# Kernel optimization log

Measured on AMD Instinct MI355X. Metric: run time of the kernel, lower is better.

Reference implementation:

```python
import jax, jax.numpy as jnp
import numpy as np

LN_EPS = 1e-5

def _ln(x, w, b):
    mu = jnp.mean(x, axis=-1, keepdims=True)
    var = jnp.var(x, axis=-1, keepdims=True)
    return (x - mu) * jax.lax.rsqrt(var + LN_EPS) * w + b

def setup_inputs() -> dict:
    key = jax.random.key(0)
    ks = jax.random.split(key, 16)
    B, T, N = 32, 1024, 77
    D, TD, TE = 512, 256, 2048
    s = lambda fan: 1.0 / np.sqrt(fan)
    return {
        "x": jax.random.normal(ks[0], (B, T, D), jnp.float32),
        "xf": jax.random.normal(ks[1], (B, N, TD), jnp.float32),
        "emb": jax.random.normal(ks[2], (B, TE), jnp.float32),
        "src_mask": jnp.ones((B, T), jnp.float32),
        "cond_type": jax.random.randint(ks[3], (B,), 0, 100, jnp.int64),
        "norm_w": jnp.ones((D,), jnp.float32),
        "norm_b": jnp.zeros((D,), jnp.float32),
        "tnorm_w": jnp.ones((TD,), jnp.float32),
        "tnorm_b": jnp.zeros((TD,), jnp.float32),
        "Wq": jax.random.normal(ks[4], (D, D), jnp.float32) * s(D),
        "bq": jnp.zeros((D,), jnp.float32),
        "Wk": jax.random.normal(ks[5], (D, TD), jnp.float32) * s(TD),
        "bk": jnp.zeros((D,), jnp.float32),
        "Wv": jax.random.normal(ks[6], (D, TD), jnp.float32) * s(TD),
        "bv": jnp.zeros((D,), jnp.float32),
        "emb_w": jax.random.normal(ks[7], (2 * D, TE), jnp.float32) * s(TE),
        "emb_b": jnp.zeros((2 * D,), jnp.float32),
        "snorm_w": jnp.ones((D,), jnp.float32),
        "snorm_b": jnp.zeros((D,), jnp.float32),
        "Wout": jax.random.normal(ks[8], (D, D), jnp.float32) * s(D),
        "bout": jnp.zeros((D,), jnp.float32),
    }

def reference(x, xf, emb, src_mask, cond_type,
              norm_w, norm_b, tnorm_w, tnorm_b,
              Wq, bq, Wk, bk, Wv, bv,
              emb_w, emb_b, snorm_w, snorm_b, Wout, bout):
    B, T, D = x.shape
    N = xf.shape[1]
    H = 8
    dh = D // H
    # projections (no 1/sqrt(dh) scaling, per original)
    q = (_ln(x, norm_w, norm_b) @ Wq.T + bq).reshape(B, T, H, dh)
    xf_n = _ln(xf, tnorm_w, tnorm_b)
    k = (xf_n @ Wk.T + bk).reshape(B, N, H, dh)
    # cond_type gating: text_cond_type = (cond_type % 10 > 0)
    tc = (cond_type % 10 > 0).astype(x.dtype)  # [B]
    bias = (1.0 - tc)[:, None, None, None] * -1000000.0  # [B,1,1,1]
    attn = jnp.einsum('bthd,bnhd->btnh', q, k) + bias
    attn = jax.nn.softmax(attn, axis=2)  # over keys N
    v = (xf_n @ Wv.T + bv) * tc[:, None, None]
    v = v.reshape(B, N, H, dh)
    y = jnp.einsum('btnh,bnhd->bthd', attn, v).reshape(B, T, D)
    # StylizationBlock: silu->linear on emb -> scale/shift, ln, silu->linear, residual
    e = jax.nn.silu(emb) @ emb_w.T + emb_b  # [B, 2D]
    scale, shift = jnp.split(e[:, None, :], 2, axis=2)  # [B,1,D] each
    h = _ln(y, snorm_w, snorm_b) * (1.0 + scale) + shift
    h = jax.nn.silu(h) @ Wout.T + bout
    return x + h
```

## Files before the change

kernel.cpp:

```cpp
#include <hip/hip_runtime.h>
#include <math.h>

#define B_   32
#define T_   1024
#define N_   77
#define D_   512
#define TD_  256
#define TE_  2048
#define H_   8
#define DH_  64

typedef short bf16x8 __attribute__((ext_vector_type(8)));
typedef float f32x4  __attribute__((ext_vector_type(4)));

__device__ __forceinline__ float sigmoidf_fast(float x) {
    return 1.0f / (1.0f + __expf(-x));
}

__device__ __forceinline__ unsigned short f2b(float f) {
    unsigned int u = __float_as_uint(f);
    unsigned int r = u + 0x7FFFu + ((u >> 16) & 1u);
    return (unsigned short)(r >> 16);
}

#define GL16(g, l) __builtin_amdgcn_global_load_lds(                         \
    (const __attribute__((address_space(1))) unsigned int*)(g),              \
    (__attribute__((address_space(3))) unsigned int*)(l), 16, 0, 0)

__global__ __launch_bounds__(256) void ln_rows_kernel(
    const float* __restrict__ x, const float* __restrict__ w, const float* __restrict__ b,
    float* __restrict__ out, int rows, int cols)
{
    int wave = blockIdx.x * 4 + (threadIdx.x >> 6);
    int lane = threadIdx.x & 63;
    if (wave >= rows) return;
    const float* row = x + (size_t)wave * cols;
    float s = 0.f, ss = 0.f;
    for (int c = lane; c < cols; c += 64) {
        float v = row[c];
        s += v; ss += v * v;
    }
    #pragma unroll
    for (int off = 32; off; off >>= 1) {
        s  += __shfl_xor(s, off);
        ss += __shfl_xor(ss, off);
    }
    float m = s / cols;
    float var = ss / cols - m * m;
    float r = rsqrtf(var + 1e-5f);
    float* orow = out + (size_t)wave * cols;
    for (int c = lane; c < cols; c += 64) {
        orow[c] = (row[c] - m) * r * w[c] + b[c];
    }
}

template <int MODE>
__global__ __launch_bounds__(256) void gemm_kernel(
    const float* __restrict__ A, const float* __restrict__ W,
    const float* __restrict__ bias,
    const int*   __restrict__ cond,
    float* __restrict__ C,
    int M, int NN, int K)
{
    const int tx = threadIdx.x & 15;
    const int ty = threadIdx.x >> 4;
    const int m0 = blockIdx.y * 64;
    const int n0 = blockIdx.x * 64;

    __shared__ float As[16][68];
    __shared__ float Ws[16][68];

    float acc[4][4] = {};

    for (int k0 = 0; k0 < K; k0 += 16) {
        int kk = k0 + tx;
        #pragma unroll
        for (int p = 0; p < 4; p++) {
            int row = ty + p * 16;
            int m = m0 + row;
            int mc = m < M ? m : (M - 1);
            As[tx][row] = A[(size_t)mc * K + kk];
        }
        #pragma unroll
        for (int p = 0; p < 4; p++) {
            int nn = ty + p * 16;
            Ws[tx][nn] = W[(size_t)(n0 + nn) * K + kk];
        }
        __syncthreads();
        #pragma unroll
        for (int cc = 0; cc < 16; cc++) {
            float4 av = *(const float4*)&As[cc][ty * 4];
            float4 wv = *(const float4*)&Ws[cc][tx * 4];
            float a4[4] = {av.x, av.y, av.z, av.w};
            float w4[4] = {wv.x, wv.y, wv.z, wv.w};
            #pragma unroll
            for (int i = 0; i < 4; i++)
                #pragma unroll
                for (int j = 0; j < 4; j++)
                    acc[i][j] = fmaf(a4[i], w4[j], acc[i][j]);
        }
        __syncthreads();
    }

    #pragma unroll
    for (int i = 0; i < 4; i++) {
        int m = m0 + ty * 4 + i;
        if (m >= M) continue;
        float rowscale = 1.f;
        if (MODE == 3) {
            int b3 = m / N_;
            rowscale = ((cond[b3] % 10) > 0) ? 1.f : 0.f;
        }
        #pragma unroll
        for (int j = 0; j < 4; j++) {
            int n = n0 + tx * 4 + j;
            float o = acc[i][j] + bias[n];
            if (MODE == 3) o *= rowscale;
            C[(size_t)m * NN + n] = o;
        }
    }
}

__global__ __launch_bounds__(256) void f32_to_bf16_kernel(
    const float* __restrict__ src, unsigned short* __restrict__ dst)
{
    int idx = (blockIdx.x * 256 + threadIdx.x) * 8;
    float4 v0 = *(const float4*)(src + idx);
    float4 v1 = *(const float4*)(src + idx + 4);
    ushort4 o0 = {f2b(v0.x), f2b(v0.y), f2b(v0.z), f2b(v0.w)};
    ushort4 o1 = {f2b(v1.x), f2b(v1.y), f2b(v1.z), f2b(v1.w)};
    *(ushort4*)(dst + idx)     = o0;
    *(ushort4*)(dst + idx + 4) = o1;
}

__global__ __launch_bounds__(256) void silu_kernel(
    const float* __restrict__ src, float* __restrict__ dst)
{
    int idx = (blockIdx.x * 256 + threadIdx.x) * 4;
    float4 v = *(const float4*)(src + idx);
    v.x = v.x * sigmoidf_fast(v.x);
    v.y = v.y * sigmoidf_fast(v.y);
    v.z = v.z * sigmoidf_fast(v.z);
    v.w = v.w * sigmoidf_fast(v.w);
    *(float4*)(dst + idx) = v;
}

__global__ __launch_bounds__(256) void emb_gemm_kernel(
    const float* __restrict__ se, const float* __restrict__ W,
    float* __restrict__ e)
{
    int wid = blockIdx.x * 4 + (threadIdx.x >> 6);
    int lane = threadIdx.x & 63;
    int ngrp = wid >> 3;
    int bgrp = wid & 7;

    float acc[4][4] = {};
    #pragma unroll 2
    for (int it = 0; it < 8; it++) {
        int k = (it * 64 + lane) * 4;
        float4 sv[4], wv[4];
        #pragma unroll
        for (int bi = 0; bi < 4; bi++)
            sv[bi] = *(const float4*)&se[(size_t)(bgrp * 4 + bi) * TE_ + k];
        #pragma unroll
        for (int ni = 0; ni < 4; ni++)
            wv[ni] = *(const float4*)&W[(size_t)(ngrp * 4 + ni) * TE_ + k];
        #pragma unroll
        for (int bi = 0; bi < 4; bi++)
            #pragma unroll
            for (int ni = 0; ni < 4; ni++) {
                acc[bi][ni] = fmaf(sv[bi].x, wv[ni].x, acc[bi][ni]);
                acc[bi][ni] = fmaf(sv[bi].y, wv[ni].y, acc[bi][ni]);
                acc[bi][ni] = fmaf(sv[bi].z, wv[ni].z, acc[bi][ni]);
                acc[bi][ni] = fmaf(sv[bi].w, wv[ni].w, acc[bi][ni]);
            }
    }
    #pragma unroll
    for (int bi = 0; bi < 4; bi++)
        #pragma unroll
        for (int ni = 0; ni < 4; ni++) {
            float a = acc[bi][ni];
            #pragma unroll
            for (int off = 32; off; off >>= 1) a += __shfl_xor(a, off);
            if (lane == 0)
                e[(size_t)(bgrp * 4 + bi) * 1024 + ngrp * 4 + ni] = a;
        }
}

__global__ __launch_bounds__(256) void prep_q_kernel(
    const float* __restrict__ x, const float* __restrict__ w, const float* __restrict__ b,
    unsigned short* __restrict__ outb)
{
    int row = blockIdx.x * 4 + (threadIdx.x >> 6);
    int lane = threadIdx.x & 63;
    const float* rp = x + (size_t)row * D_ + lane * 8;
    float4 v0 = *(const float4*)rp;
    float4 v1 = *(const float4*)(rp + 4);
    float s  = v0.x + v0.y + v0.z + v0.w + v1.x + v1.y + v1.z + v1.w;
    float ss = v0.x*v0.x + v0.y*v0.y + v0.z*v0.z + v0.w*v0.w
             + v1.x*v1.x + v1.y*v1.y + v1.z*v1.z + v1.w*v1.w;
    #pragma unroll
    for (int off = 32; off; off >>= 1) {
        s  += __shfl_xor(s, off);
        ss += __shfl_xor(ss, off);
    }
    float m = s * (1.f / D_);
    float r = rsqrtf(ss * (1.f / D_) - m * m + 1e-5f);
    float4 w0 = *(const float4*)(w + lane * 8);
    float4 w1 = *(const float4*)(w + lane * 8 + 4);
    float4 b0 = *(const float4*)(b + lane * 8);
    float4 b1 = *(const float4*)(b + lane * 8 + 4);
    ushort4 o0, o1;
    o0.x = f2b((v0.x - m) * r * w0.x + b0.x);
    o0.y = f2b((v0.y - m) * r * w0.y + b0.y);
    o0.z = f2b((v0.z - m) * r * w0.z + b0.z);
    o0.w = f2b((v0.w - m) * r * w0.w + b0.w);
    o1.x = f2b((v1.x - m) * r * w1.x + b1.x);
    o1.y = f2b((v1.y - m) * r * w1.y + b1.y);
    o1.z = f2b((v1.z - m) * r * w1.z + b1.z);
    o1.w = f2b((v1.w - m) * r * w1.w + b1.w);
    unsigned short* op = outb + (size_t)row * D_ + lane * 8;
    *(ushort4*)op       = o0;
    *(ushort4*)(op + 4) = o1;
}

__global__ __launch_bounds__(256) void prep_h_kernel(
    const float* __restrict__ y, const float* __restrict__ w, const float* __restrict__ b,
    const float* __restrict__ e, const float* __restrict__ emb_b,
    unsigned short* __restrict__ outb)
{
    int row = blockIdx.x * 4 + (threadIdx.x >> 6);
    int lane = threadIdx.x & 63;
    int bb = row >> 10;
    const float* rp = y + (size_t)row * D_ + lane * 8;
    float4 v0 = *(const float4*)rp;
    float4 v1 = *(const float4*)(rp + 4);
    float s  = v0.x + v0.y + v0.z + v0.w + v1.x + v1.y + v1.z + v1.w;
    float ss = v0.x*v0.x + v0.y*v0.y + v0.z*v0.z + v0.w*v0.w
             + v1.x*v1.x + v1.y*v1.y + v1.z*v1.z + v1.w*v1.w;
    #pragma unroll
    for (int off = 32; off; off >>= 1) {
        s  += __shfl_xor(s, off);
        ss += __shfl_xor(ss, off);
    }
    float m = s * (1.f / D_);
    float r = rsqrtf(ss * (1.f / D_) - m * m + 1e-5f);
    float4 w0 = *(const float4*)(w + lane * 8);
    float4 w1 = *(const float4*)(w + lane * 8 + 4);
    float4 b0 = *(const float4*)(b + lane * 8);
    float4 b1 = *(const float4*)(b + lane * 8 + 4);
    const float* ep = e + (size_t)bb * 1024 + lane * 8;
    float4 sc0 = *(const float4*)ep;
    float4 sc1 = *(const float4*)(ep + 4);
    float4 sh0 = *(const float4*)(ep + 512);
    float4 sh1 = *(const float4*)(ep + 512 + 4);
    float4 eb0 = *(const float4*)(emb_b + lane * 8);
    float4 eb1 = *(const float4*)(emb_b + lane * 8 + 4);
    float4 fb0 = *(const float4*)(emb_b + 512 + lane * 8);
    float4 fb1 = *(const float4*)(emb_b + 512 + lane * 8 + 4);
    sc0.x += eb0.x; sc0.y += eb0.y; sc0.z += eb0.z; sc0.w += eb0.w;
    sc1.x += eb1.x; sc1.y += eb1.y; sc1.z += eb1.z; sc1.w += eb1.w;
    sh0.x += fb0.x; sh0.y += fb0.y; sh0.z += fb0.z; sh0.w += fb0.w;
    sh1.x += fb1.x; sh1.y += fb1.y; sh1.z += fb1.z; sh1.w += fb1.w;
    float hv[8];
    hv[0] = ((v0.x - m) * r * w0.x + b0.x) * (1.f + sc0.x) + sh0.x;
    hv[1] = ((v0.y - m) * r * w0.y + b0.y) * (1.f + sc0.y) + sh0.y;
    hv[2] = ((v0.z - m) * r * w0.z + b0.z) * (1.f + sc0.z) + sh0.z;
    hv[3] = ((v0.w - m) * r * w0.w + b0.w) * (1.f + sc0.w) + sh0.w;
    hv[4] = ((v1.x - m) * r * w1.x + b1.x) * (1.f + sc1.x) + sh1.x;
    hv[5] = ((v1.y - m) * r * w1.y + b1.y) * (1.f + sc1.y) + sh1.y;
    hv[6] = ((v1.z - m) * r * w1.z + b1.z) * (1.f + sc1.z) + sh1.z;
    hv[7] = ((v1.w - m) * r * w1.w + b1.w) * (1.f + sc1.w) + sh1.w;
    ushort4 o0, o1;
    o0.x = f2b(hv[0] * sigmoidf_fast(hv[0]));
    o0.y = f2b(hv[1] * sigmoidf_fast(hv[1]));
    o0.z = f2b(hv[2] * sigmoidf_fast(hv[2]));
    o0.w = f2b(hv[3] * sigmoidf_fast(hv[3]));
    o1.x = f2b(hv[4] * sigmoidf_fast(hv[4]));
    o1.y = f2b(hv[5] * sigmoidf_fast(hv[5]));
    o1.z = f2b(hv[6] * sigmoidf_fast(hv[6]));
    o1.w = f2b(hv[7] * sigmoidf_fast(hv[7]));
    unsigned short* op = outb + (size_t)row * D_ + lane * 8;
    *(ushort4*)op       = o0;
    *(ushort4*)(op + 4) = o1;
}

template <int RESID, int OUTBF>
__global__ __launch_bounds__(256) void gemm_bf16_kernel(
    const unsigned short* __restrict__ Ab,
    const unsigned short* __restrict__ Wb,
    const float* __restrict__ bias,
    const float* __restrict__ resid,
    void* __restrict__ Cv)
{
    constexpr int K = 512;
    __shared__ __align__(16) unsigned short As[128 * 32];
    __shared__ __align__(16) unsigned short Bs[128 * 32];

    const int tid  = threadIdx.x;
    const int m0   = blockIdx.y * 128;
    const int n0   = blockIdx.x * 128;
    const int lane = tid & 63;
    const int w    = tid >> 6;
    const int l15  = lane & 15;
    const int quad = lane >> 4;
    const int wm   = (w >> 1) * 64;
    const int wn   = (w & 1) * 64;

    const int row_a = tid >> 2;
    const int col16 = tid & 3;

    f32x4 acc[4][4];
    #pragma unroll
    for (int i = 0; i < 4; i++)
        #pragma unroll
        for (int j = 0; j < 4; j++)
            acc[i][j] = (f32x4){0.f, 0.f, 0.f, 0.f};

    const char* gAbase = (const char*)Ab + ((size_t)(m0 + row_a) * K) * 2 + col16 * 16;
    const char* gBbase = (const char*)Wb + ((size_t)(n0 + row_a) * K) * 2 + col16 * 16;
    char* lA = (char*)As + tid * 16;
    char* lB = (char*)Bs + tid * 16;

    for (int k0 = 0; k0 < K; k0 += 32) {
        const char* gA = gAbase + k0 * 2;
        const char* gB = gBbase + k0 * 2;
        GL16(gA, lA);
        GL16(gA + (size_t)64 * K * 2, lA + 4096);
        GL16(gB, lB);
        GL16(gB + (size_t)64 * K * 2, lB + 4096);
        __syncthreads();

        bf16x8 af[4], bfr[4];
        #pragma unroll
        for (int i = 0; i < 4; i++)
            af[i] = *(const bf16x8*)&As[(wm + i * 16 + l15) * 32 + quad * 8];
        #pragma unroll
        for (int j = 0; j < 4; j++)
            bfr[j] = *(const bf16x8*)&Bs[(wn + j * 16 + l15) * 32 + quad * 8];
        #pragma unroll
        for (int i = 0; i < 4; i++)
            #pragma unroll
            for (int j = 0; j < 4; j++)
                acc[i][j] = __builtin_amdgcn_mfma_f32_16x16x32_bf16(af[i], bfr[j], acc[i][j], 0, 0, 0);
        __syncthreads();
    }

    float* C = (float*)Cv;
    unsigned short* Cb = (unsigned short*)Cv;
    #pragma unroll
    for (int i = 0; i < 4; i++) {
        int mbase = m0 + wm + i * 16 + quad * 4;
        #pragma unroll
        for (int j = 0; j < 4; j++) {
            int n = n0 + wn + j * 16 + l15;
            float bn = bias[n];
            #pragma unroll
            for (int r = 0; r < 4; r++) {
                size_t off = (size_t)(mbase + r) * 512 + n;
                float v = acc[i][j][r] + bn;
                if (RESID) v += resid[off];
                if (OUTBF) Cb[off] = f2b(v);
                else       C[off]  = v;
            }
        }
    }
}

#define QS_OFF 0
#define KS_OFF 4608
#define VT_OFF 10368
#define PS_OFF 17024
#define SMEM_SH 23680

__global__ __launch_bounds__(256) void attn_mfma_kernel(
    const unsigned short* __restrict__ qb,
    const float* __restrict__ kbuf, const float* __restrict__ vbuf,
    float* __restrict__ yout)
{
    __shared__ __align__(16) unsigned short smem[SMEM_SH];

    const int tid = threadIdx.x;
    const int t0 = blockIdx.x * 64;
    const int h  = blockIdx.y;
    const int b  = blockIdx.z;

    const unsigned short* qbase = qb + ((size_t)(b * T_ + t0)) * D_ + h * 64;
    #pragma unroll
    for (int i = 0; i < 2; i++) {
        int idx = tid + i * 256;
        int row = idx >> 3, c8 = idx & 7;
        bf16x8 v = *(const bf16x8*)(qbase + (size_t)row * D_ + c8 * 8);
        *(bf16x8*)&smem[QS_OFF + row * 72 + c8 * 8] = v;
    }
    const float* kbase = kbuf + (size_t)(b * N_) * D_ + h * 64;
    #pragma unroll
    for (int i = 0; i < 5; i++) {
        int idx = tid + i * 256;
        if (idx < N_ * 16) {
            int row = idx >> 4, c4 = idx & 15;
            float4 v = *(const float4*)(kbase + (size_t)row * D_ + c4 * 4);
            ushort4 o;
            o.x = f2b(v.x); o.y = f2b(v.y); o.z = f2b(v.z); o.w = f2b(v.w);
            *(ushort4*)&smem[KS_OFF + row * 72 + c4 * 4] = o;
        }
    }
    if (tid < 48) {
        int row = N_ + tid / 16, c4 = tid & 15;
        ushort4 z = {0, 0, 0, 0};
        *(ushort4*)&smem[KS_OFF + row * 72 + c4 * 4] = z;
    }
    const float* vbase = vbuf + (size_t)(b * N_) * D_ + h * 64;
    #pragma unroll
    for (int i = 0; i < 5; i++) {
        int idx = tid + i * 256;
        if (idx < N_ * 16) {
            int n = idx >> 4, c4 = idx & 15;
            float4 v = *(const float4*)(vbase + (size_t)n * D_ + c4 * 4);
            smem[VT_OFF + (c4 * 4 + 0) * 104 + n] = f2b(v.x);
            smem[VT_OFF + (c4 * 4 + 1) * 104 + n] = f2b(v.y);
            smem[VT_OFF + (c4 * 4 + 2) * 104 + n] = f2b(v.z);
            smem[VT_OFF + (c4 * 4 + 3) * 104 + n] = f2b(v.w);
        }
    }
    #pragma unroll
    for (int i = 0; i < 5; i++) {
        int idx = tid + i * 256;
        if (idx < 64 * 19) {
            int d = idx / 19, n = N_ + idx % 19;
            smem[VT_OFF + d * 104 + n] = 0;
        }
    }
    #pragma unroll
    for (int i = 0; i < 4; i++) {
        int idx = tid + i * 256;
        int row = idx >> 4, col = 80 + (idx & 15);
        smem[PS_OFF + row * 104 + col] = 0;
    }
    __syncthreads();

    const int lane = tid & 63;
    const int w    = tid >> 6;
    const int l15  = lane & 15;
    const int quad = lane >> 4;
    const int koff = quad * 8;
    const int mrow = w * 16 + l15;

    bf16x8 aq0 = *(const bf16x8*)&smem[QS_OFF + mrow * 72 + koff];
    bf16x8 aq1 = *(const bf16x8*)&smem[QS_OFF + mrow * 72 + 32 + koff];

    float s[5][4];
    #pragma unroll
    for (int nt = 0; nt < 5; nt++) {
        bf16x8 bk0 = *(const bf16x8*)&smem[KS_OFF + (nt * 16 + l15) * 72 + koff];
        bf16x8 bk1 = *(const bf16x8*)&smem[KS_OFF + (nt * 16 + l15) * 72 + 32 + koff];
        f32x4 c = {0.f, 0.f, 0.f, 0.f};
        c = __builtin_amdgcn_mfma_f32_16x16x32_bf16(aq0, bk0, c, 0, 0, 0);
        c = __builtin_amdgcn_mfma_f32_16x16x32_bf16(aq1, bk1, c, 0, 0, 0);
        #pragma unroll
        for (int r = 0; r < 4; r++) s[nt][r] = c[r];
    }
    if (l15 >= N_ - 64) {
        #pragma unroll
        for (int r = 0; r < 4; r++) s[4][r] = -1e30f;
    }
    float li[4];
    #pragma unroll
    for (int r = 0; r < 4; r++) {
        float m = s[0][r];
        #pragma unroll
        for (int nt = 1; nt < 5; nt++) m = fmaxf(m, s[nt][r]);
        m = fmaxf(m, __shfl_xor(m, 1));
        m = fmaxf(m, __shfl_xor(m, 2));
        m = fmaxf(m, __shfl_xor(m, 4));
        m = fmaxf(m, __shfl_xor(m, 8));
        float l = 0.f;
        #pragma unroll
        for (int nt = 0; nt < 5; nt++) {
            float ev = __expf(s[nt][r] - m);
            s[nt][r] = ev;
            l += ev;
        }
        l += __shfl_xor(l, 1);
        l += __shfl_xor(l, 2);
        l += __shfl_xor(l, 4);
        l += __shfl_xor(l, 8);
        li[r] = 1.f / l;
    }
    #pragma unroll
    for (int r = 0; r < 4; r++) {
        int prow = w * 16 + quad * 4 + r;
        #pragma unroll
        for (int nt = 0; nt < 5; nt++) {
            smem[PS_OFF + prow * 104 + nt * 16 + l15] = f2b(s[nt][r] * li[r]);
        }
    }

    bf16x8 pa0 = *(const bf16x8*)&smem[PS_OFF + mrow * 104 + 0  + koff];
    bf16x8 pa1 = *(const bf16x8*)&smem[PS_OFF + mrow * 104 + 32 + koff];
    bf16x8 pa2 = *(const bf16x8*)&smem[PS_OFF + mrow * 104 + 64 + koff];

    float* obase = yout + ((size_t)(b * T_ + t0 + w * 16)) * D_ + h * 64;
    #pragma unroll
    for (int dt = 0; dt < 4; dt++) {
        bf16x8 bv0 = *(const bf16x8*)&smem[VT_OFF + (dt * 16 + l15) * 104 + 0  + koff];
        bf16x8 bv1 = *(const bf16x8*)&smem[VT_OFF + (dt * 16 + l15) * 104 + 32 + koff];
        bf16x8 bv2 = *(const bf16x8*)&smem[VT_OFF + (dt * 16 + l15) * 104 + 64 + koff];
        f32x4 c = {0.f, 0.f, 0.f, 0.f};
        c = __builtin_amdgcn_mfma_f32_16x16x32_bf16(pa0, bv0, c, 0, 0, 0);
        c = __builtin_amdgcn_mfma_f32_16x16x32_bf16(pa1, bv1, c, 0, 0, 0);
        c = __builtin_amdgcn_mfma_f32_16x16x32_bf16(pa2, bv2, c, 0, 0, 0);
        #pragma unroll
        for (int r = 0; r < 4; r++) {
            obase[(size_t)(quad * 4 + r) * D_ + dt * 16 + l15] = c[r];
        }
    }
}

extern "C" void kernel_launch(void* const* d_in, const int* in_sizes, int n_in,
                              void* d_out, int out_size, void* d_ws, size_t ws_size,
                              hipStream_t stream)
{
    const float* x       = (const float*)d_in[0];
    const float* xf      = (const float*)d_in[1];
    const float* emb     = (const float*)d_in[2];
    const int*   cond    = (const int*)d_in[4];
    const float* norm_w  = (const float*)d_in[5];
    const float* norm_b  = (const float*)d_in[6];
    const float* tnorm_w = (const float*)d_in[7];
    const float* tnorm_b = (const float*)d_in[8];
    const float* Wq      = (const float*)d_in[9];
    const float* bq      = (const float*)d_in[10];
    const float* Wk      = (const float*)d_in[11];
    const float* bk      = (const float*)d_in[12];
    const float* Wv      = (const float*)d_in[13];
    const float* bv      = (const float*)d_in[14];
    const float* emb_w   = (const float*)d_in[15];
    const float* emb_b   = (const float*)d_in[16];
    const float* snorm_w = (const float*)d_in[17];
    const float* snorm_b = (const float*)d_in[18];
    const float* Wout    = (const float*)d_in[19];
    const float* bout    = (const float*)d_in[20];
    float* out = (float*)d_out;

    float* ws = (float*)d_ws;
    float* qy   = ws;
    float* xfn  = qy   + (size_t)B_ * T_ * D_;
    float* kbuf = xfn  + (size_t)B_ * N_ * TD_;
    float* vbuf = kbuf + (size_t)B_ * N_ * D_;
    float* ebuf = vbuf + (size_t)B_ * N_ * D_;
    float* sebuf= ebuf + (size_t)B_ * 2 * D_;
    unsigned short* abh = (unsigned short*)(sebuf + (size_t)B_ * TE_);
    unsigned short* wqb = abh + (size_t)B_ * T_ * D_;
    unsigned short* wob = wqb + (size_t)D_ * D_;
    unsigned short* qb  = (unsigned short*)d_out;

    const int BT = B_ * T_;
    const int BN = B_ * N_;

    ln_rows_kernel<<<(BN + 3) / 4, 256, 0, stream>>>(xf, tnorm_w, tnorm_b, xfn, BN, TD_);
    {
        dim3 grid(D_ / 64, (BN + 63) / 64);
        gemm_kernel<2><<<grid, 256, 0, stream>>>(xfn, Wk, bk, nullptr, kbuf, BN, D_, TD_);
    }
    {
        dim3 grid(D_ / 64, (BN + 63) / 64);
        gemm_kernel<3><<<grid, 256, 0, stream>>>(xfn, Wv, bv, cond, vbuf, BN, D_, TD_);
    }
    f32_to_bf16_kernel<<<128, 256, 0, stream>>>(Wq, wqb);
    f32_to_bf16_kernel<<<128, 256, 0, stream>>>(Wout, wob);
    prep_q_kernel<<<BT / 4, 256, 0, stream>>>(x, norm_w, norm_b, abh);
    {
        dim3 grid(D_ / 128, BT / 128);
        gemm_bf16_kernel<0, 1><<<grid, 256, 0, stream>>>(abh, wqb, bq, nullptr, qb);
    }
    silu_kernel<<<(B_ * TE_) / 1024, 256, 0, stream>>>(emb, sebuf);
    emb_gemm_kernel<<<512, 256, 0, stream>>>(sebuf, emb_w, ebuf);
    {
        dim3 grid(T_ / 64, H_, B_);
        attn_mfma_kernel<<<grid, 256, 0, stream>>>(qb, kbuf, vbuf, qy);
    }
    prep_h_kernel<<<BT / 4, 256, 0, stream>>>(qy, snorm_w, snorm_b, ebuf, emb_b, abh);
    {
        dim3 grid(D_ / 128, BT / 128);
        gemm_bf16_kernel<1, 0><<<grid, 256, 0, stream>>>(abh, wob, bout, x, out);
    }
}
```

Before: 346.7 us.

## Move K/V projection to bf16 MFMA GEMM and fuse small prep kernels

Replaces the two fp32 SIMT K and V GEMMs with a single bf16 MFMA GEMM that computes K and V together from a bf16 layer-normed xf and writes bf16 outputs. It also merges the weight conversions into one launch and folds SiLU into the embedding GEMM. The attention kernel now reads bf16 K/V directly, loads Q straight into registers, and uses an XOR-swizzled transposed V layout in shared memory. These changes cut launch count, fp32 traffic and per-block conversion work, at the cost of reduced K/V precision and more complex indexing. The LN xf buffer is padded to 2560 rows, but rows beyond 2464 are never written and are read uninitialised, though those results are discarded.

```diff
diff --git a/kernel.cpp b/kernel.cpp
--- a/kernel.cpp
+++ b/kernel.cpp
@@ -27,104 +27,46 @@
     (const __attribute__((address_space(1))) unsigned int*)(g),              \
     (__attribute__((address_space(3))) unsigned int*)(l), 16, 0, 0)
 
-__global__ __launch_bounds__(256) void ln_rows_kernel(
+__global__ __launch_bounds__(256) void ln_xf_kernel(
     const float* __restrict__ x, const float* __restrict__ w, const float* __restrict__ b,
-    float* __restrict__ out, int rows, int cols)
-{
-    int wave = blockIdx.x * 4 + (threadIdx.x >> 6);
+    unsigned short* __restrict__ outb)
+{
+    int row = blockIdx.x * 4 + (threadIdx.x >> 6);
     int lane = threadIdx.x & 63;
-    if (wave >= rows) return;
-    const float* row = x + (size_t)wave * cols;
-    float s = 0.f, ss = 0.f;
-    for (int c = lane; c < cols; c += 64) {
-        float v = row[c];
-        s += v; ss += v * v;
-    }
+    const float* rp = x + (size_t)row * TD_ + lane * 4;
+    float4 v = *(const float4*)rp;
+    float s  = v.x + v.y + v.z + v.w;
+    float ss = v.x*v.x + v.y*v.y + v.z*v.z + v.w*v.w;
     #pragma unroll
     for (int off = 32; off; off >>= 1) {
         s  += __shfl_xor(s, off);
         ss += __shfl_xor(ss, off);
     }
-    float m = s / cols;
-    float var = ss / cols - m * m;
-    float r = rsqrtf(var + 1e-5f);
-    float* orow = out + (size_t)wave * cols;
-    for (int c = lane; c < cols; c += 64) {
-        orow[c] = (row[c] - m) * r * w[c] + b[c];
-    }
-}
-
-template <int MODE>
-__global__ __launch_bounds__(256) void gemm_kernel(
-    const float* __restrict__ A, const float* __restrict__ W,
-    const float* __restrict__ bias,
-    const int*   __restrict__ cond,
-    float* __restrict__ C,
-    int M, int NN, int K)
-{
-    const int tx = threadIdx.x & 15;
-    const int ty = threadIdx.x >> 4;
-    const int m0 = blockIdx.y * 64;
-    const int n0 = blockIdx.x * 64;
-
-    __shared__ float As[16][68];
-    __shared__ float Ws[16][68];
-
-    float acc[4][4] = {};
-
-    for (int k0 = 0; k0 < K; k0 += 16) {
-        int kk = k0 + tx;
-        #pragma unroll
-        for (int p = 0; p < 4; p++) {
-            int row = ty + p * 16;
-            int m = m0 + row;
-            int mc = m < M ? m : (M - 1);
-            As[tx][row] = A[(size_t)mc * K + kk];
-        }
-        #pragma unroll
-        for (int p = 0; p < 4; p++) {
-            int nn = ty + p * 16;
-            Ws[tx][nn] = W[(size_t)(n0 + nn) * K + kk];
-        }
-        __syncthreads();
-        #pragma unroll
-        for (int cc = 0; cc < 16; cc++) {
-            float4 av = *(const float4*)&As[cc][ty * 4];
-            float4 wv = *(const float4*)&Ws[cc][tx * 4];
-            float a4[4] = {av.x, av.y, av.z, av.w};
-            float w4[4] = {wv.x, wv.y, wv.z, wv.w};
-            #pragma unroll
-            for (int i = 0; i < 4; i++)
-                #pragma unroll
-                for (int j = 0; j < 4; j++)
-                    acc[i][j] = fmaf(a4[i], w4[j], acc[i][j]);
-        }
-        __syncthreads();
-    }
-
-    #pragma unroll
-    for (int i = 0; i < 4; i++) {
-        int m = m0 + ty * 4 + i;
-        if (m >= M) continue;
-        float rowscale = 1.f;
-        if (MODE == 3) {
-            int b3 = m / N_;
-            rowscale = ((cond[b3] % 10) > 0) ? 1.f : 0.f;
-        }
-        #pragma unroll
-        for (int j = 0; j < 4; j++) {
-            int n = n0 + tx * 4 + j;
-            float o = acc[i][j] + bias[n];
-            if (MODE == 3) o *= rowscale;
-            C[(size_t)m * NN + n] = o;
-        }
-    }
-}
-
-__global__ __launch_bounds__(256) void f32_to_bf16_kernel(
-    const float* __restrict__ src, unsigned short* __restrict__ dst)
-{
-    int idx = (blockIdx.x * 256 + threadIdx.x) * 8;
+    float m = s * (1.f / TD_);
+    float r = rsqrtf(ss * (1.f / TD_) - m * m + 1e-5f);
+    float4 wv = *(const float4*)(w + lane * 4);
+    float4 bv = *(const float4*)(b + lane * 4);
+    ushort4 o;
+    o.x = f2b((v.x - m) * r * wv.x + bv.x);
+    o.y = f2b((v.y - m) * r * wv.y + bv.y);
+    o.z = f2b((v.z - m) * r * wv.z + bv.z);
+    o.w = f2b((v.w - m) * r * wv.w + bv.w);
+    *(ushort4*)(outb + (size_t)row * TD_ + lane * 4) = o;
+}
+
+__global__ __launch_bounds__(256) void conv_weights_kernel(
+    const float* __restrict__ Wq, const float* __restrict__ Wout,
+    const float* __restrict__ Wk, const float* __restrict__ Wv,
+    unsigned short* __restrict__ wqb, unsigned short* __restrict__ wob,
+    unsigned short* __restrict__ wkvb)
+{
+    int bid = blockIdx.x;
+    const float* src; unsigned short* dst;
+    if (bid < 128)      { src = Wq;   dst = wqb; }
+    else if (bid < 256) { src = Wout; dst = wob;               bid -= 128; }
+    else if (bid < 320) { src = Wk;   dst = wkvb;              bid -= 256; }
+    else                { src = Wv;   dst = wkvb + D_ * TD_;   bid -= 320; }
+    int idx = (bid * 256 + threadIdx.x) * 8;
     float4 v0 = *(const float4*)(src + idx);
     float4 v1 = *(const float4*)(src + idx + 4);
     ushort4 o0 = {f2b(v0.x), f2b(v0.y), f2b(v0.z), f2b(v0.w)};
@@ -133,20 +75,93 @@
     *(ushort4*)(dst + idx + 4) = o1;
 }
 
-__global__ __launch_bounds__(256) void silu_kernel(
-    const float* __restrict__ src, float* __restrict__ dst)
-{
-    int idx = (blockIdx.x * 256 + threadIdx.x) * 4;
-    float4 v = *(const float4*)(src + idx);
-    v.x = v.x * sigmoidf_fast(v.x);
-    v.y = v.y * sigmoidf_fast(v.y);
-    v.z = v.z * sigmoidf_fast(v.z);
-    v.w = v.w * sigmoidf_fast(v.w);
-    *(float4*)(dst + idx) = v;
+__global__ __launch_bounds__(256) void kv_gemm_kernel(
+    const unsigned short* __restrict__ Ab,
+    const unsigned short* __restrict__ Wb,
+    const float* __restrict__ bkp, const float* __restrict__ bvp,
+    const int*   __restrict__ cond,
+    unsigned short* __restrict__ kout, unsigned short* __restrict__ vout)
+{
+    constexpr int K = TD_;
+    __shared__ __align__(16) unsigned short As[128 * 32];
+    __shared__ __align__(16) unsigned short Bs[128 * 32];
+
+    const int tid  = threadIdx.x;
+    const int m0   = blockIdx.y * 128;
+    const int n0   = blockIdx.x * 128;
+    const int lane = tid & 63;
+    const int w    = tid >> 6;
+    const int l15  = lane & 15;
+    const int quad = lane >> 4;
+    const int wm   = (w >> 1) * 64;
+    const int wn   = (w & 1) * 64;
+
+    const int row_a = tid >> 2;
+    const int col16 = tid & 3;
+
+    f32x4 acc[4][4];
+    #pragma unroll
+    for (int i = 0; i < 4; i++)
+        #pragma unroll
+        for (int j = 0; j < 4; j++)
+            acc[i][j] = (f32x4){0.f, 0.f, 0.f, 0.f};
+
+    const char* gAbase = (const char*)Ab + ((size_t)(m0 + row_a) * K) * 2 + col16 * 16;
+    const char* gBbase = (const char*)Wb + ((size_t)(n0 + row_a) * K) * 2 + col16 * 16;
+    char* lA = (char*)As + tid * 16;
+    char* lB = (char*)Bs + tid * 16;
+
+    for (int k0 = 0; k0 < K; k0 += 32) {
+        const char* gA = gAbase + k0 * 2;
+        const char* gB = gBbase + k0 * 2;
+        GL16(gA, lA);
+        GL16(gA + (size_t)64 * K * 2, lA + 4096);
+        GL16(gB, lB);
+        GL16(gB + (size_t)64 * K * 2, lB + 4096);
+        __syncthreads();
+
+        bf16x8 af[4], bfr[4];
+        #pragma unroll
+        for (int i = 0; i < 4; i++)
+            af[i] = *(const bf16x8*)&As[(wm + i * 16 + l15) * 32 + quad * 8];
+        #pragma unroll
+        for (int j = 0; j < 4; j++)
+            bfr[j] = *(const bf16x8*)&Bs[(wn + j * 16 + l15) * 32 + quad * 8];
+        #pragma unroll
+        for (int i = 0; i < 4; i++)
+            #pragma unroll
+            for (int j = 0; j < 4; j++)
+                acc[i][j] = __builtin_amdgcn_mfma_f32_16x16x32_bf16(af[i], bfr[j], acc[i][j], 0, 0, 0);
+        __syncthreads();
+    }
+
+    #pragma unroll
+    for (int i = 0; i < 4; i++) {
+        int mbase = m0 + wm + i * 16 + quad * 4;
+        #pragma unroll
+        for (int j = 0; j < 4; j++) {
+            int n = n0 + wn + j * 16 + l15;
+            bool isv = n >= D_;
+            int nn = isv ? n - D_ : n;
+            float bn = isv ? bvp[nn] : bkp[nn];
+            unsigned short* outp = isv ? vout : kout;
+            #pragma unroll
+            for (int r = 0; r < 4; r++) {
+                int m = mbase + r;
+                if (m >= B_ * N_) continue;
+                float v = acc[i][j][r] + bn;
+                if (isv) {
+                    int bi = m / N_;
+                    v = ((cond[bi] % 10) > 0) ? v : 0.f;
+                }
+                outp[(size_t)m * D_ + nn] = f2b(v);
+            }
+        }
+    }
 }
 
 __global__ __launch_bounds__(256) void emb_gemm_kernel(
-    const float* __restrict__ se, const float* __restrict__ W,
+    const float* __restrict__ emb, const float* __restrict__ W,
     float* __restrict__ e)
 {
     int wid = blockIdx.x * 4 + (threadIdx.x >> 6);
@@ -160,8 +175,14 @@
         int k = (it * 64 + lane) * 4;
         float4 sv[4], wv[4];
         #pragma unroll
-        for (int bi = 0; bi < 4; bi++)
-            sv[bi] = *(const float4*)&se[(size_t)(bgrp * 4 + bi) * TE_ + k];
+        for (int bi = 0; bi < 4; bi++) {
+            float4 t = *(const float4*)&emb[(size_t)(bgrp * 4 + bi) * TE_ + k];
+            t.x *= sigmoidf_fast(t.x);
+            t.y *= sigmoidf_fast(t.y);
+            t.z *= sigmoidf_fast(t.z);
+            t.w *= sigmoidf_fast(t.w);
+            sv[bi] = t;
+        }
         #pragma unroll
         for (int ni = 0; ni < 4; ni++)
             wv[ni] = *(const float4*)&W[(size_t)(ngrp * 4 + ni) * TE_ + k];
@@ -367,77 +388,23 @@
     }
 }
 
-#define QS_OFF 0
-#define KS_OFF 4608
-#define VT_OFF 10368
-#define PS_OFF 17024
-#define SMEM_SH 23680
-
-__global__ __launch_bounds__(256) void attn_mfma_kernel(
+#define KS2   0
+#define VT2   5760
+#define PS2   11904
+#define SMEM2 18560
+
+__global__ __launch_bounds__(256) void attn_mfma2_kernel(
     const unsigned short* __restrict__ qb,
-    const float* __restrict__ kbuf, const float* __restrict__ vbuf,
+    const unsigned short* __restrict__ kb,
+    const unsigned short* __restrict__ vb,
     float* __restrict__ yout)
 {
-    __shared__ __align__(16) unsigned short smem[SMEM_SH];
+    __shared__ __align__(16) unsigned short smem[SMEM2];
 
     const int tid = threadIdx.x;
     const int t0 = blockIdx.x * 64;
     const int h  = blockIdx.y;
     const int b  = blockIdx.z;
-
-    const unsigned short* qbase = qb + ((size_t)(b * T_ + t0)) * D_ + h * 64;
-    #pragma unroll
-    for (int i = 0; i < 2; i++) {
-        int idx = tid + i * 256;
-        int row = idx >> 3, c8 = idx & 7;
-        bf16x8 v = *(const bf16x8*)(qbase + (size_t)row * D_ + c8 * 8);
-        *(bf16x8*)&smem[QS_OFF + row * 72 + c8 * 8] = v;
-    }
-    const float* kbase = kbuf + (size_t)(b * N_) * D_ + h * 64;
-    #pragma unroll
-    for (int i = 0; i < 5; i++) {
-        int idx = tid + i * 256;
-        if (idx < N_ * 16) {
-            int row = idx >> 4, c4 = idx & 15;
-            float4 v = *(const float4*)(kbase + (size_t)row * D_ + c4 * 4);
-            ushort4 o;
-            o.x = f2b(v.x); o.y = f2b(v.y); o.z = f2b(v.z); o.w = f2b(v.w);
-            *(ushort4*)&smem[KS_OFF + row * 72 + c4 * 4] = o;
-        }
-    }
-    if (tid < 48) {
-        int row = N_ + tid / 16, c4 = tid & 15;
-        ushort4 z = {0, 0, 0, 0};
-        *(ushort4*)&smem[KS_OFF + row * 72 + c4 * 4] = z;
-    }
-    const float* vbase = vbuf + (size_t)(b * N_) * D_ + h * 64;
-    #pragma unroll
-    for (int i = 0; i < 5; i++) {
-        int idx = tid + i * 256;
-        if (idx < N_ * 16) {
-            int n = idx >> 4, c4 = idx & 15;
-            float4 v = *(const float4*)(vbase + (size_t)n * D_ + c4 * 4);
-            smem[VT_OFF + (c4 * 4 + 0) * 104 + n] = f2b(v.x);
-            smem[VT_OFF + (c4 * 4 + 1) * 104 + n] = f2b(v.y);
-            smem[VT_OFF + (c4 * 4 + 2) * 104 + n] = f2b(v.z);
-            smem[VT_OFF + (c4 * 4 + 3) * 104 + n] = f2b(v.w);
-        }
-    }
-    #pragma unroll
-    for (int i = 0; i < 5; i++) {
-        int idx = tid + i * 256;
-        if (idx < 64 * 19) {
-            int d = idx / 19, n = N_ + idx % 19;
-            smem[VT_OFF + d * 104 + n] = 0;
-        }
-    }
-    #pragma unroll
-    for (int i = 0; i < 4; i++) {
-        int idx = tid + i * 256;
-        int row = idx >> 4, col = 80 + (idx & 15);
-        smem[PS_OFF + row * 104 + col] = 0;
-    }
-    __syncthreads();
 
     const int lane = tid & 63;
     const int w    = tid >> 6;
@@ -446,14 +413,62 @@
     const int koff = quad * 8;
     const int mrow = w * 16 + l15;
 
-    bf16x8 aq0 = *(const bf16x8*)&smem[QS_OFF + mrow * 72 + koff];
-    bf16x8 aq1 = *(const bf16x8*)&smem[QS_OFF + mrow * 72 + 32 + koff];
+    const unsigned short* qrow = qb + ((size_t)(b * T_ + t0 + mrow)) * D_ + h * 64 + koff;
+    bf16x8 aq0 = *(const bf16x8*)qrow;
+    bf16x8 aq1 = *(const bf16x8*)(qrow + 32);
+
+    const unsigned short* kbase = kb + ((size_t)(b * N_)) * D_ + h * 64;
+    #pragma unroll
+    for (int i = 0; i < 3; i++) {
+        int idx = tid + i * 256;
+        if (idx < 640) {
+            int row = idx >> 3, c8 = idx & 7;
+            bf16x8 v = (bf16x8){0, 0, 0, 0, 0, 0, 0, 0};
+            if (row < N_) v = *(const bf16x8*)(kbase + (size_t)row * D_ + c8 * 8);
+            *(bf16x8*)&smem[KS2 + row * 72 + c8 * 8] = v;
+        }
+    }
+    const unsigned short* vbase = vb + ((size_t)(b * N_)) * D_ + h * 64;
+    #pragma unroll
+    for (int i = 0; i < 3; i++) {
+        int idx = tid + i * 256;
+        if (idx < 616) {
+            int n = idx >> 3, c8 = idx & 7;
+            bf16x8 v = *(const bf16x8*)(vbase + (size_t)n * D_ + c8 * 8);
+            int cn = n >> 3, wn = n & 7;
+            #pragma unroll
+            for (int j = 0; j < 8; j++) {
+                int d = c8 * 8 + j;
+                int s2 = (j ^ c8) & 3;
+                smem[VT2 + d * 96 + ((cn ^ s2) << 3) + wn] = v[j];
+            }
+        }
+    }
+    if (tid < 128) {
+        int d = tid >> 1, c = 10 + (tid & 1);
+        int s2 = (d ^ (d >> 3)) & 3;
+        *(bf16x8*)&smem[VT2 + d * 96 + ((c ^ s2) << 3)] = (bf16x8){0, 0, 0, 0, 0, 0, 0, 0};
+    }
+    {
+        int d = tid >> 2, t = tid & 3;
+        if (t < 3) {
+            int s2 = (d ^ (d >> 3)) & 3;
+            smem[VT2 + d * 96 + ((9 ^ s2) << 3) + 5 + t] = 0;
+        }
+    }
+    #pragma unroll
+    for (int i = 0; i < 4; i++) {
+        int idx = tid + i * 256;
+        int row = idx >> 4, col = 80 + (idx & 15);
+        smem[PS2 + row * 104 + col] = 0;
+    }
+    __syncthreads();
 
     float s[5][4];
     #pragma unroll
     for (int nt = 0; nt < 5; nt++) {
-        bf16x8 bk0 = *(const bf16x8*)&smem[KS_OFF + (nt * 16 + l15) * 72 + koff];
-        bf16x8 bk1 = *(const bf16x8*)&smem[KS_OFF + (nt * 16 + l15) * 72 + 32 + koff];
+        bf16x8 bk0 = *(const bf16x8*)&smem[KS2 + (nt * 16 + l15) * 72 + koff];
+        bf16x8 bk1 = *(const bf16x8*)&smem[KS2 + (nt * 16 + l15) * 72 + 32 + koff];
         f32x4 c = {0.f, 0.f, 0.f, 0.f};
         c = __builtin_amdgcn_mfma_f32_16x16x32_bf16(aq0, bk0, c, 0, 0, 0);
         c = __builtin_amdgcn_mfma_f32_16x16x32_bf16(aq1, bk1, c, 0, 0, 0);
@@ -492,20 +507,22 @@
         int prow = w * 16 + quad * 4 + r;
         #pragma unroll
         for (int nt = 0; nt < 5; nt++) {
-            smem[PS_OFF + prow * 104 + nt * 16 + l15] = f2b(s[nt][r] * li[r]);
-        }
-    }
-
-    bf16x8 pa0 = *(const bf16x8*)&smem[PS_OFF + mrow * 104 + 0  + koff];
-    bf16x8 pa1 = *(const bf16x8*)&smem[PS_OFF + mrow * 104 + 32 + koff];
-    bf16x8 pa2 = *(const bf16x8*)&smem[PS_OFF + mrow * 104 + 64 + koff];
+            smem[PS2 + prow * 104 + nt * 16 + l15] = f2b(s[nt][r] * li[r]);
+        }
+    }
+
+    bf16x8 pa0 = *(const bf16x8*)&smem[PS2 + mrow * 104 + 0  + koff];
+    bf16x8 pa1 = *(const bf16x8*)&smem[PS2 + mrow * 104 + 32 + koff];
+    bf16x8 pa2 = *(const bf16x8*)&smem[PS2 + mrow * 104 + 64 + koff];
 
     float* obase = yout + ((size_t)(b * T_ + t0 + w * 16)) * D_ + h * 64;
     #pragma unroll
     for (int dt = 0; dt < 4; dt++) {
-        bf16x8 bv0 = *(const bf16x8*)&smem[VT_OFF + (dt * 16 + l15) * 104 + 0  + koff];
-        bf16x8 bv1 = *(const bf16x8*)&smem[VT_OFF + (dt * 16 + l15) * 104 + 32 + koff];
-        bf16x8 bv2 = *(const bf16x8*)&smem[VT_OFF + (dt * 16 + l15) * 104 + 64 + koff];
+        int drow = dt * 16 + l15;
+        int s2 = (drow ^ (drow >> 3)) & 3;
+        bf16x8 bv0 = *(const bf16x8*)&smem[VT2 + drow * 96 + (((0 + quad) ^ s2) << 3)];
+        bf16x8 bv1 = *(const bf16x8*)&smem[VT2 + drow * 96 + (((4 + quad) ^ s2) << 3)];
+        bf16x8 bv2 = *(const bf16x8*)&smem[VT2 + drow * 96 + (((8 + quad) ^ s2) << 3)];
         f32x4 c = {0.f, 0.f, 0.f, 0.f};
         c = __builtin_amdgcn_mfma_f32_16x16x32_bf16(pa0, bv0, c, 0, 0, 0);
         c = __builtin_amdgcn_mfma_f32_16x16x32_bf16(pa1, bv1, c, 0, 0, 0);
@@ -545,40 +562,35 @@
 
     float* ws = (float*)d_ws;
     float* qy   = ws;
-    float* xfn  = qy   + (size_t)B_ * T_ * D_;
-    float* kbuf = xfn  + (size_t)B_ * N_ * TD_;
-    float* vbuf = kbuf + (size_t)B_ * N_ * D_;
-    float* ebuf = vbuf + (size_t)B_ * N_ * D_;
-    float* sebuf= ebuf + (size_t)B_ * 2 * D_;
-    unsigned short* abh = (unsigned short*)(sebuf + (size_t)B_ * TE_);
-    unsigned short* wqb = abh + (size_t)B_ * T_ * D_;
-    unsigned short* wob = wqb + (size_t)D_ * D_;
-    unsigned short* qb  = (unsigned short*)d_out;
+    float* ebuf = qy + (size_t)B_ * T_ * D_;
+    unsigned short* u = (unsigned short*)(ebuf + (size_t)B_ * 2 * D_);
+    unsigned short* xfnb = u;  u += (size_t)2560 * TD_;
+    unsigned short* kb16 = u;  u += (size_t)B_ * N_ * D_;
+    unsigned short* vb16 = u;  u += (size_t)B_ * N_ * D_;
+    unsigned short* abh  = u;  u += (size_t)B_ * T_ * D_;
+    unsigned short* wqb  = u;  u += (size_t)D_ * D_;
+    unsigned short* wob  = u;  u += (size_t)D_ * D_;
+    unsigned short* wkvb = u;  u += (size_t)2 * D_ * TD_;
+    unsigned short* qb = (unsigned short*)d_out;
 
     const int BT = B_ * T_;
     const int BN = B_ * N_;
 
-    ln_rows_kernel<<<(BN + 3) / 4, 256, 0, stream>>>(xf, tnorm_w, tnorm_b, xfn, BN, TD_);
+    ln_xf_kernel<<<BN / 4, 256, 0, stream>>>(xf, tnorm_w, tnorm_b, xfnb);
+    conv_weights_kernel<<<384, 256, 0, stream>>>(Wq, Wout, Wk, Wv, wqb, wob, wkvb);
     {
-        dim3 grid(D_ / 64, (BN + 63) / 64);
-        gemm_kernel<2><<<grid, 256, 0, stream>>>(xfn, Wk, bk, nullptr, kbuf, BN, D_, TD_);
-    }
-    {
-        dim3 grid(D_ / 64, (BN + 63) / 64);
-        gemm_kernel<3><<<grid, 256, 0, stream>>>(xfn, Wv, bv, cond, vbuf, BN, D_, TD_);
-    }
-    f32_to_bf16_kernel<<<128, 256, 0, stream>>>(Wq, wqb);
-    f32_to_bf16_kernel<<<128, 256, 0, stream>>>(Wout, wob);
+        dim3 grid(1024 / 128, 2560 / 128);
+        kv_gemm_kernel<<<grid, 256, 0, stream>>>(xfnb, wkvb, bk, bv, cond, kb16, vb16);
+    }
     prep_q_kernel<<<BT / 4, 256, 0, stream>>>(x, norm_w, norm_b, abh);
     {
         dim3 grid(D_ / 128, BT / 128);
         gemm_bf16_kernel<0, 1><<<grid, 256, 0, stream>>>(abh, wqb, bq, nullptr, qb);
     }
-    silu_kernel<<<(B_ * TE_) / 1024, 256, 0, stream>>>(emb, sebuf);
-    emb_gemm_kernel<<<512, 256, 0, stream>>>(sebuf, emb_w, ebuf);
+    emb_gemm_kernel<<<512, 256, 0, stream>>>(emb, emb_w, ebuf);
     {
         dim3 grid(T_ / 64, H_, B_);
-        attn_mfma_kernel<<<grid, 256, 0, stream>>>(qb, kbuf, vbuf, qy);
+        attn_mfma2_kernel<<<grid, 256, 0, stream>>>(qb, kb16, vb16, qy);
     }
     prep_h_kernel<<<BT / 4, 256, 0, stream>>>(qy, snorm_w, snorm_b, ebuf, emb_b, abh);
     {
```

New measurement: 316.2 us. 1.1x faster.
